# Kernel optimization log

Measured on AMD Instinct MI355X. Metric: run time of the kernel, lower is better.

## Reference

```python
import jax, jax.numpy as jnp
import numpy as np

V, E, H, T = 50000, 1024, 1024, 128
L, MAXL = 50, 50
PAD, O_TOK = 0, 1


def setup_inputs() -> dict:
    key = jax.random.key(0)
    ks = jax.random.split(key, 18)
    s = 0.05
    f = lambda k, shape: jax.random.normal(k, shape, jnp.float32) * s
    return {
        'input_ids': jax.random.randint(ks[0], (1, L), 1, V),
        'tag_ids': jax.random.randint(ks[1], (1, L), 1, T),  # >=1 so no pad tags
        'word_embed': f(ks[2], (V, E)),
        'enc_Wih': f(ks[3], (3 * H, E)),
        'enc_Whh': f(ks[4], (3 * H, H)),
        'enc_bih': f(ks[5], (3 * H,)),
        'enc_bhh': f(ks[6], (3 * H,)),
        'dec_embed': f(ks[7], (T, H)),
        'attn_W': f(ks[8], (MAXL, 2 * H)),
        'attn_b': f(ks[9], (MAXL,)),
        'comb_W': f(ks[10], (H, 2 * H)),
        'comb_b': f(ks[11], (H,)),
        'dec_Wih': f(ks[12], (3 * H, H)),
        'dec_Whh': f(ks[13], (3 * H, H)),
        'dec_bih': f(ks[14], (3 * H,)),
        'dec_bhh': f(ks[15], (3 * H,)),
        'out_W': f(ks[16], (T, H)),
        'out_b': f(ks[17], (T,)),
    }


def _gru_cell(x, h, Wih, Whh, bih, bhh):
    # PyTorch GRU cell semantics
    gi = Wih @ x + bih
    gh = Whh @ h + bhh
    i_r, i_z, i_n = jnp.split(gi, 3)
    h_r, h_z, h_n = jnp.split(gh, 3)
    r = jax.nn.sigmoid(i_r + h_r)
    z = jax.nn.sigmoid(i_z + h_z)
    n = jnp.tanh(i_n + r * h_n)
    return (1.0 - z) * n + z * h


def _forward(word_embed, enc_Wih, enc_Whh, enc_bih, enc_bhh,
             dec_embed, attn_W, attn_b, comb_W, comb_b,
             dec_Wih, dec_Whh, dec_bih, dec_bhh, out_W, out_b,
             input_ids, tag_ids):
    src = input_ids[0]  # (L,)
    tgt = tag_ids[0]    # (L,)

    def enc_step(h, tok):
        h2 = _gru_cell(word_embed[tok], h, enc_Wih, enc_Whh, enc_bih, enc_bhh)
        return h2, h2

    h_enc, enc_outs = jax.lax.scan(enc_step, jnp.zeros((H,), word_embed.dtype), src)
    # enc_outs: (L, H); L == MAX_LENGTH so the buffer is fully filled

    dec_in = jnp.concatenate([jnp.array([O_TOK], tgt.dtype), tgt[:-1]])  # teacher forcing

    def dec_step(h, xt):
        tok, tgt_t = xt
        e = dec_embed[tok]  # (H,), dropout is identity in eval
        aw = jax.nn.softmax(attn_W @ jnp.concatenate([e, h]) + attn_b)  # (MAXL,)
        ctx = aw @ enc_outs  # (H,)
        o = jax.nn.relu(comb_W @ jnp.concatenate([e, ctx]) + comb_b)
        h2 = _gru_cell(o, h, dec_Wih, dec_Whh, dec_bih, dec_bhh)
        logp = jax.nn.log_softmax(out_W @ h2 + out_b)  # decoder output (log-probs)
        # original applies CrossEntropyLoss on log-probs -> log_softmax applied twice
        nll = -jax.nn.log_softmax(logp)[tgt_t]
        step_loss = jnp.where(tgt_t == PAD, jnp.zeros((), logp.dtype), nll)
        return h2, (logp, step_loss)

    _, (logps, losses) = jax.lax.scan(dec_step, h_enc, (dec_in, tgt))
    return logps, jnp.sum(losses)  # (L, T), scalar


def reference(input_ids, tag_ids, word_embed, enc_Wih, enc_Whh, enc_bih, enc_bhh,
              dec_embed, attn_W, attn_b, comb_W, comb_b,
              dec_Wih, dec_Whh, dec_bih, dec_bhh, out_W, out_b):
    return _forward(word_embed, enc_Wih, enc_Whh, enc_bih, enc_bhh,
                    dec_embed, attn_W, attn_b, comb_W, comb_b,
                    dec_Wih, dec_Whh, dec_bih, dec_bhh, out_W, out_b,
                    input_ids, tag_ids)
```

## Files before the change

### kernel.cpp

```cpp
#include <hip/hip_runtime.h>
#include <cstdint>


#define HDIM 1024
#define LSEQ 50
#define TDIM 128
#define PB   6
#define NPROD 128
#define LSTRP 65

typedef float f32x4 __attribute__((ext_vector_type(4)));
typedef _Float16 h2 __attribute__((ext_vector_type(2)));

#if __has_builtin(__builtin_amdgcn_fdot2)
#define FDOT2(a,b,c) __builtin_amdgcn_fdot2((a),(b),(c),false)
#else
__device__ __forceinline__ float fdot2_sw(h2 a, h2 b, float c){
  return c + (float)a[0]*(float)b[0] + (float)a[1]*(float)b[1];
}
#define FDOT2(a,b,c) fdot2_sw((a),(b),(c))
#endif

struct KArgs {
  const int* input_ids; const int* tag_ids;
  const float* word_embed;
  const float* enc_Wih; const float* enc_Whh; const float* enc_bih; const float* enc_bhh;
  const float* dec_embed; const float* attn_W; const float* attn_b;
  const float* comb_W; const float* comb_b;
  const float* dec_Wih; const float* dec_Whh; const float* dec_bih; const float* dec_bhh;
  const float* out_W; const float* out_b;
  float* out;
  unsigned* ctrE; unsigned* ctrM; unsigned* ctrO; unsigned* ctrV;
  float* hbE;
  float* hbD;
  float* obD;
  float* logits;
  float* attn_e;
  float* pre_comb;
  float* MT;
  float* enc_outs;
};

__device__ __forceinline__ void fence_vm(){
  asm volatile("s_waitcnt vmcnt(0)" ::: "memory");
}
__device__ __forceinline__ void st_coh(float* p, float v){
  __hip_atomic_store(p, v, __ATOMIC_RELAXED, __HIP_MEMORY_SCOPE_AGENT);
}
__device__ __forceinline__ void st_tag(float* p, float v, unsigned tag){
  unsigned b = (__float_as_uint(v) & ~31u) | tag;
  st_coh(p, __uint_as_float(b));
}
__device__ __forceinline__ void stf(unsigned* p, unsigned v){
  __hip_atomic_store(p, v, __ATOMIC_RELAXED, __HIP_MEMORY_SCOPE_AGENT);
}
__device__ __forceinline__ unsigned ldu(const unsigned* p){
  return __hip_atomic_load(p, __ATOMIC_RELAXED, __HIP_MEMORY_SCOPE_AGENT);
}
__device__ __forceinline__ void addc(unsigned* base, int bid){
  __hip_atomic_fetch_add(base + (bid&7)*16, 1u, __ATOMIC_RELAXED, __HIP_MEMORY_SCOPE_AGENT);
}
__device__ __forceinline__ void addc0(unsigned* base){
  __hip_atomic_fetch_add(base, 1u, __ATOMIC_RELAXED, __HIP_MEMORY_SCOPE_AGENT);
}
__device__ __forceinline__ f32x4 coh_load4(const float* p){
  f32x4 v;
  asm volatile("global_load_dwordx4 %0, %1, off sc0 sc1\n\ts_waitcnt vmcnt(0)"
               : "=v"(v) : "v"(p) : "memory");
  return v;
}

template<int N>
__device__ __forceinline__ void wred_batch(float* v){
  #pragma unroll
  for(int o=32;o>0;o>>=1){
    #pragma unroll
    for(int i=0;i<N;i++) v[i] += __shfl_xor(v[i],o,64);
  }
}
__device__ __forceinline__ float wred_sum(float v){
  #pragma unroll
  for(int o=32;o>0;o>>=1) v += __shfl_xor(v,o,64);
  return v;
}
__device__ __forceinline__ float wred_max(float v){
  #pragma unroll
  for(int o=32;o>0;o>>=1) v = fmaxf(v,__shfl_xor(v,o,64));
  return v;
}

struct Chunk { f32x4 a,b,c,d; };
__device__ __forceinline__ Chunk load_chunk(const float* __restrict__ row, int lane){
  const f32x4* p = reinterpret_cast<const f32x4*>(row) + lane*4;
  Chunk w; w.a=p[0]; w.b=p[1]; w.c=p[2]; w.d=p[3]; return w;
}
__device__ __forceinline__ float chunk_dot(const Chunk& w, const float* hc){
  return w.a.x*hc[0]+w.a.y*hc[1]+w.a.z*hc[2]+w.a.w*hc[3]
       + w.b.x*hc[4]+w.b.y*hc[5]+w.b.z*hc[6]+w.b.w*hc[7]
       + w.c.x*hc[8]+w.c.y*hc[9]+w.c.z*hc[10]+w.c.w*hc[11]
       + w.d.x*hc[12]+w.d.y*hc[13]+w.d.z*hc[14]+w.d.w*hc[15];
}
__device__ __forceinline__ void load_vec16(const float* __restrict__ v, float* hc, int lane){
  const f32x4* p = reinterpret_cast<const f32x4*>(v) + lane*4;
  f32x4 x0=p[0],x1=p[1],x2=p[2],x3=p[3];
  hc[0]=x0.x; hc[1]=x0.y; hc[2]=x0.z; hc[3]=x0.w;
  hc[4]=x1.x; hc[5]=x1.y; hc[6]=x1.z; hc[7]=x1.w;
  hc[8]=x2.x; hc[9]=x2.y; hc[10]=x2.z; hc[11]=x2.w;
  hc[12]=x3.x; hc[13]=x3.y; hc[14]=x3.z; hc[15]=x3.w;
}

struct PChunk { unsigned m[8]; };
__device__ __forceinline__ h2 as_h2(unsigned u){ return __builtin_bit_cast(h2, u); }
__device__ __forceinline__ unsigned as_u(h2 h){ return __builtin_bit_cast(unsigned, h); }
__device__ __forceinline__ unsigned pack2(float a, float b){
  return as_u((h2){(_Float16)a, (_Float16)b});
}
__device__ __forceinline__ PChunk load_pchunk(const float* __restrict__ row, int lane){
  const f32x4* p = reinterpret_cast<const f32x4*>(row) + lane*4;
  f32x4 a=p[0],b=p[1],c=p[2],d=p[3];
  PChunk w;
  w.m[0]=pack2(a.x,a.y); w.m[1]=pack2(a.z,a.w);
  w.m[2]=pack2(b.x,b.y); w.m[3]=pack2(b.z,b.w);
  w.m[4]=pack2(c.x,c.y); w.m[5]=pack2(c.z,c.w);
  w.m[6]=pack2(d.x,d.y); w.m[7]=pack2(d.z,d.w);
  return w;
}
__device__ __forceinline__ void pinp(PChunk& c){
  asm volatile("" : "+v"(c.m[0]),"+v"(c.m[1]),"+v"(c.m[2]),"+v"(c.m[3]),
                    "+v"(c.m[4]),"+v"(c.m[5]),"+v"(c.m[6]),"+v"(c.m[7]));
}
__device__ __forceinline__ void pin32(unsigned& x){ asm volatile("" : "+v"(x)); }
__device__ __forceinline__ float pdot(const PChunk& w, const h2* hp){
  float acc = 0.f;
  #pragma unroll
  for(int k=0;k<8;k++) acc = FDOT2(as_h2(w.m[k]), hp[k], acc);
  return acc;
}
__device__ __forceinline__ float sigm(float x){ return 1.f/(1.f+expf(-x)); }
__device__ __forceinline__ void pack16(const float* ec, h2* ep){
  #pragma unroll
  for(int k=0;k<8;k++) ep[k]=(h2){(_Float16)ec[2*k],(_Float16)ec[2*k+1]};
}

template<int SLP>
__device__ __forceinline__ void stage_tag_p(h2* ldsp, const float* g, int tid, unsigned tag){
  const float* p = g + 4*tid;
  f32x4 v;
  for(;;){
    v = coh_load4(p);
    unsigned m = ((__float_as_uint(v.x)&31u)^tag) | ((__float_as_uint(v.y)&31u)^tag)
               | ((__float_as_uint(v.z)&31u)^tag) | ((__float_as_uint(v.w)&31u)^tag);
    if(m==0u) break;
    if(SLP) __builtin_amdgcn_s_sleep(SLP);
  }
  int q = tid>>2, m0 = (tid&3)*2;
  ldsp[m0*LSTRP+q]     = (h2){(_Float16)v.x,(_Float16)v.y};
  ldsp[(m0+1)*LSTRP+q] = (h2){(_Float16)v.z,(_Float16)v.w};
}
__device__ __forceinline__ void read8p(const h2* ldsp, h2* hp, int lane){
  #pragma unroll
  for(int k=0;k<8;k++) hp[k]=ldsp[k*LSTRP+lane];
}
__device__ __forceinline__ float hread(const h2* ldsp, int j){
  int pj = j>>1;
  h2 v = ldsp[(pj&7)*LSTRP + (pj>>3)];
  return (float)v[j&1];
}

__device__ __forceinline__ void wait8(const unsigned* base, unsigned n, int lane){
  const unsigned* p = base + lane*16;
  for(;;){
    unsigned v = (lane<8)? ldu(p) : 0xFFFFFFFFu;
    if(__all((int)(v>=n))) return;
    __builtin_amdgcn_s_sleep(8);
  }
}

__global__ __launch_bounds__(256,1) void seq2seq_kernel(KArgs A){
  const int bid = blockIdx.x, tid = threadIdx.x;
  const int wave = tid>>6, lane = tid&63;
  __shared__ h2 ldsp_h[8*LSTRP+8];
  __shared__ h2 ldsp_o[8*LSTRP+8];
  __shared__ h2 awpL[32];
  __shared__ float smr[64];
  __shared__ float smL[TDIM];
  __shared__ float smA[64];
  __shared__ float giL[LSEQ*24];

  const int gv = bid*4 + wave;

  const int p = bid - PB;
  const bool is_prod = (p>=0 && p<NPROD);
  const int base = is_prod ? p*8 : 0;
  const int j8 = base + (tid&7);

  if(is_prod){
    {
      PChunk wgi[6]; float bgi[6];
      #pragma unroll
      for(int i=0;i<6;i++){
        int r = wave + 4*i;
        int le=r/3, g=r-3*le, grow=g*HDIM+base+le;
        wgi[i] = load_pchunk(A.enc_Wih + (size_t)grow*HDIM, lane);
        pinp(wgi[i]);
        bgi[i] = A.enc_bih[grow];
      }
      for(int te=0;te<LSEQ;++te){
        int tok = A.input_ids[te];
        float ec[16]; load_vec16(A.word_embed + (size_t)tok*HDIM, ec, lane);
        h2 ep[8]; pack16(ec, ep);
        float d[6];
        #pragma unroll
        for(int i=0;i<6;i++) d[i]=pdot(wgi[i],ep);
        wred_batch<6>(d);
        if(lane==0){
          #pragma unroll
          for(int i=0;i<6;i++) giL[te*24 + wave+4*i] = d[i]+bgi[i];
        }
      }
      __syncthreads();
    }
    PChunk wep[6];
    #pragma unroll
    for(int i=0;i<6;i++){
      int r = wave + 4*i;
      int le=r/3, g=r-3*le, row=g*HDIM+base+le;
      wep[i] = load_pchunk(A.enc_Whh + (size_t)row*HDIM, lane);
      pinp(wep[i]);
    }
    float bh0=A.enc_bhh[j8], bh1=A.enc_bhh[HDIM+j8], bh2=A.enc_bhh[2*HDIM+j8];
    for(int te=0;te<LSEQ;++te){
      h2 hp[8];
      if(te>0){
        stage_tag_p<1>(ldsp_h, A.hbE + ((te-1)&1)*HDIM, tid, (unsigned)(te&31));
        __syncthreads();
        read8p(ldsp_h, hp, lane);
      } else {
        #pragma unroll
        for(int k=0;k<8;k++) hp[k]=(h2){(_Float16)0.f,(_Float16)0.f};
      }
      float part[6];
      #pragma unroll
      for(int i=0;i<6;i++) part[i]=pdot(wep[i],hp);
      wred_batch<6>(part);
      if(lane==0){
        #pragma unroll
        for(int i=0;i<6;i++) smr[wave+4*i]=part[i];
      }
      __syncthreads();
      if(tid<8){
        int j = base+tid;
        float gr=smr[tid*3]+bh0, gz=smr[tid*3+1]+bh1, gn=smr[tid*3+2]+bh2;
        float gi0=giL[te*24+3*tid], gi1=giL[te*24+3*tid+1], gi2=giL[te*24+3*tid+2];
        float hj = (te>0)? hread(ldsp_h, j) : 0.f;
        float r_=sigm(gi0+gr), z_=sigm(gi1+gz);
        float n_=tanhf(gi2+r_*gn);
        float h2v=(1.f-z_)*n_+z_*hj;
        st_tag(&A.hbE[(te&1)*HDIM+j], h2v, (unsigned)((te+1)&31));
        st_coh(&A.enc_outs[te*HDIM+j], h2v);
        if(te==LSEQ-1) st_tag(&A.hbD[j], h2v, 0u);
      }
      __syncthreads();
    }
    fence_vm();
    __syncthreads();
    if(tid==0) addc(A.ctrE, bid);
  } else {
    const int q = (bid<6)? bid : bid-128;
    PChunk wpc[2]; float bpc[2]; int ri[2];
    #pragma unroll
    for(int k=0;k<2;k++){
      ri[k] = q*8 + wave*2 + k;
      wpc[k] = load_pchunk(A.comb_W + (size_t)ri[k]*2*HDIM, lane);
      pinp(wpc[k]);
      bpc[k] = A.comb_b[ri[k]];
    }
    for(int t=0;t<LSEQ;++t){
      int tok = (t==0)?1:A.tag_ids[t-1];
      float ec[16]; load_vec16(A.dec_embed + (size_t)tok*HDIM, ec, lane);
      h2 ep[8]; pack16(ec, ep);
      float d[2] = {pdot(wpc[0],ep), pdot(wpc[1],ep)};
      wred_batch<2>(d);
      if(lane==0){
        st_coh(&A.pre_comb[t*HDIM+ri[0]], d[0]+bpc[0]);
        st_coh(&A.pre_comb[t*HDIM+ri[1]], d[1]+bpc[1]);
      }
    }
    if(q < LSEQ){
      PChunk wae = load_pchunk(A.attn_W + (size_t)q*2*HDIM, lane);
      float bae = A.attn_b[q];
      const int t0 = wave*13, tc = (wave<3)?13:11;
      for(int u=0;u<tc;++u){
        int t = t0+u;
        int tok = (t==0)?1:A.tag_ids[t-1];
        float ec[16]; load_vec16(A.dec_embed + (size_t)tok*HDIM, ec, lane);
        h2 ep[8]; pack16(ec, ep);
        float d = wred_sum(pdot(wae,ep));
        if(lane==0) st_coh(&A.attn_e[t*LSEQ+q], d+bae);
      }
    }
    fence_vm();
    __syncthreads();
  }

  if(wave==0) wait8(A.ctrE, 16u, lane);
  __syncthreads();
  {
    Chunk wm = load_chunk(A.comb_W + (size_t)gv*2*HDIM + HDIM, lane);
    for(int sg=0;sg<10;++sg){
      float pt[5];
      #pragma unroll
      for(int j=0;j<5;j++){
        float ec[16]; load_vec16(A.enc_outs + (sg*5+j)*HDIM, ec, lane);
        pt[j]=chunk_dot(wm,ec);
      }
      wred_batch<5>(pt);
      if(lane==0){
        #pragma unroll
        for(int j=0;j<5;j++) st_coh(&A.MT[(sg*5+j)*HDIM+gv], pt[j]);
      }
    }
  }
  fence_vm();
  __syncthreads();
  if(tid==0) addc(A.ctrM, bid);
  {
    const bool keep = is_prod || bid<5 || (bid>=134 && bid<150);
    if(!keep) return;
  }
  if(wave==0) wait8(A.ctrM, 32u, lane);
  __syncthreads();

  if(bid < 4){
    const int oi = bid*256 + tid;
    PChunk wa13[13];
    int srow[13];
    #pragma unroll
    for(int i=0;i<13;i++){
      int s = wave + 4*i; int sc = (s<LSEQ)? s : 0;
      wa13[i] = load_pchunk(A.attn_W + (size_t)sc*2*HDIM + HDIM, lane);
      pinp(wa13[i]);
      srow[i] = s;
    }
    unsigned mp[25];
    #pragma unroll
    for(int k=0;k<25;k++){
      mp[k] = pack2(A.MT[(2*k)*HDIM+oi], A.MT[(2*k+1)*HDIM+oi]);
      pin32(mp[k]);
    }
    for(int t=0;t<LSEQ;++t){
      const unsigned tg = (unsigned)(t&31);
      float ae[13];
      #pragma unroll
      for(int i=0;i<13;i++)
        ae[i] = (srow[i]<LSEQ)? A.attn_e[t*LSEQ+srow[i]] : 0.f;
      float pcv = A.pre_comb[t*HDIM+oi];
      stage_tag_p<1>(ldsp_h, A.hbD + (t%3)*HDIM, tid, tg);
      __syncthreads();
      h2 hp[8]; read8p(ldsp_h, hp, lane);
      float pl[13];
      #pragma unroll
      for(int i=0;i<13;i++) pl[i]=pdot(wa13[i],hp);
      wred_batch<13>(pl);
      if(lane==0){
        #pragma unroll
        for(int i=0;i<13;i++) if(srow[i]<LSEQ) smL[srow[i]]=pl[i]+ae[i];
      }
      __syncthreads();
      if(wave==0){
        float l = (lane<LSEQ)? smL[lane] : -1e30f;
        float m = wred_max(l);
        float pe = (lane<LSEQ)? expf(l-m) : 0.f;
        float ss = wred_sum(pe);
        if(lane<LSEQ) smA[lane] = pe/ss;
      }
      __syncthreads();
      if(tid<25) awpL[tid] = (h2){(_Float16)smA[2*tid],(_Float16)smA[2*tid+1]};
      __syncthreads();
      float acc = pcv;
      #pragma unroll
      for(int k=0;k<25;k++) acc = FDOT2(as_h2(mp[k]), awpL[k], acc);
      st_tag(&A.obD[(t&1)*HDIM+oi], fmaxf(acc,0.f), tg);
      __syncthreads();
    }
  } else if(bid == 4){
    float loss = 0.f;
    for(int t=0;t<LSEQ;++t){
      if(tid<32){
        const float* pp = A.logits + (t&1)*TDIM + 4*tid;
        const unsigned tg = (unsigned)(t&31);
        f32x4 v;
        for(;;){
          v = coh_load4(pp);
          unsigned m = ((__float_as_uint(v.x)&31u)^tg) | ((__float_as_uint(v.y)&31u)^tg)
                     | ((__float_as_uint(v.z)&31u)^tg) | ((__float_as_uint(v.w)&31u)^tg);
          if(m==0u) break;
          __builtin_amdgcn_s_sleep(2);
        }
        smL[4*tid]=v.x; smL[4*tid+1]=v.y; smL[4*tid+2]=v.z; smL[4*tid+3]=v.w;
      }
      __syncthreads();
      if(tid==0) stf(A.ctrV, (unsigned)(t+1));
      if(wave==0){
        float l0=smL[lane], l1=smL[lane+64];
        float m  = wred_max(fmaxf(l0,l1));
        float pe = expf(l0-m)+expf(l1-m);
        float s1 = wred_sum(pe);
        float lse = m + logf(s1);
        float lp0 = l0-lse, lp1 = l1-lse;
        float m2  = wred_max(fmaxf(lp0,lp1));
        float p2  = expf(lp0-m2)+expf(lp1-m2);
        float s2  = wred_sum(p2);
        float lse2 = m2 + logf(s2);
        A.out[t*TDIM + lane]      = lp0;
        A.out[t*TDIM + 64 + lane] = lp1;
        int tg2 = A.tag_ids[t];
        float c = ((lane==tg2)?(lse2-lp0):0.f) + ((lane+64==tg2)?(lse2-lp1):0.f);
        c = wred_sum(c);
        if(tg2 != 0) loss += c;
      }
      __syncthreads();
    }
    if(tid==0) A.out[LSEQ*TDIM] = loss;
  } else if(is_prod){
    PChunk whp[6], wip[6];
    #pragma unroll
    for(int i=0;i<6;i++){
      int r = wave + 4*i;
      int le=r/3, g=r-3*le, row=g*HDIM+base+le;
      whp[i] = load_pchunk(A.dec_Whh + (size_t)row*HDIM, lane);
      pinp(whp[i]);
      wip[i] = load_pchunk(A.dec_Wih + (size_t)row*HDIM, lane);
      pinp(wip[i]);
    }
    float dh0=A.dec_bhh[j8], dh1=A.dec_bhh[HDIM+j8], dh2=A.dec_bhh[2*HDIM+j8];
    float di0=A.dec_bih[j8], di1=A.dec_bih[HDIM+j8], di2=A.dec_bih[2*HDIM+j8];
    for(int t=0;t<LSEQ;++t){
      const unsigned tg = (unsigned)(t&31);
      stage_tag_p<1>(ldsp_h, A.hbD + (t%3)*HDIM, tid, tg);
      __syncthreads();
      h2 hp[8]; read8p(ldsp_h, hp, lane);
      float ph[6];
      #pragma unroll
      for(int i=0;i<6;i++) ph[i]=pdot(whp[i],hp);
      wred_batch<6>(ph);
      if(lane==0){
        #pragma unroll
        for(int i=0;i<6;i++) smr[wave+4*i]=ph[i];
      }
      if(wave==0 && t>=3){
        const unsigned tgt = 16u*(unsigned)(t-2);
        for(;;){
          unsigned v = (lane==0)? ldu(A.ctrO) : tgt;
          if(__all((int)(v>=tgt))) break;
          __builtin_amdgcn_s_sleep(2);
        }
      }
      stage_tag_p<1>(ldsp_o, A.obD + (t&1)*HDIM, tid, tg);
      __syncthreads();
      h2 op[8]; read8p(ldsp_o, op, lane);
      float po[6];
      #pragma unroll
      for(int i=0;i<6;i++) po[i]=pdot(wip[i],op);
      wred_batch<6>(po);
      if(lane==0){
        #pragma unroll
        for(int i=0;i<6;i++) smr[32+wave+4*i]=po[i];
      }
      __syncthreads();
      if(tid<8){
        int j = base+tid;
        float gr=smr[tid*3]+dh0,    gz=smr[tid*3+1]+dh1,    gn=smr[tid*3+2]+dh2;
        float ir=smr[32+tid*3]+di0, iz=smr[32+tid*3+1]+di1, inn=smr[32+tid*3+2]+di2;
        float hj = hread(ldsp_h, j);
        float r_=sigm(ir+gr), z_=sigm(iz+gz);
        float n_=tanhf(inn+r_*gn);
        float h2v=(1.f-z_)*n_+z_*hj;
        st_tag(&A.hbD[((t+1)%3)*HDIM+j], h2v, (unsigned)((t+1)&31));
      }
      __syncthreads();
    }
  } else {
    const int ob = bid-134;
    PChunk wop[2];
    float bo[2];
    #pragma unroll
    for(int i=0;i<2;i++){
      int row = ob*8 + wave*2 + i;
      wop[i]=load_pchunk(A.out_W+(size_t)row*HDIM,lane);
      pinp(wop[i]);
      bo[i]=A.out_b[row];
    }
    for(int t=0;t<LSEQ;++t){
      const unsigned tg1 = (unsigned)((t+1)&31);
      stage_tag_p<2>(ldsp_h, A.hbD + ((t+1)%3)*HDIM, tid, tg1);
      __syncthreads();
      if(tid==0) addc0(A.ctrO);
      h2 hp[8]; read8p(ldsp_h, hp, lane);
      float pt[2]={pdot(wop[0],hp),pdot(wop[1],hp)};
      wred_batch<2>(pt);
      if(wave==0 && t>=2){
        const unsigned tgt = (unsigned)(t-1);
        for(;;){
          unsigned v = (lane==0)? ldu(A.ctrV) : tgt;
          if(__all((int)(v>=tgt))) break;
          __builtin_amdgcn_s_sleep(4);
        }
      }
      __syncthreads();
      if(lane==0){
        int row = ob*8 + wave*2;
        st_tag(&A.logits[(t&1)*TDIM + row],   pt[0]+bo[0], (unsigned)(t&31));
        st_tag(&A.logits[(t&1)*TDIM + row+1], pt[1]+bo[1], (unsigned)(t&31));
      }
      __syncthreads();
    }
  }
}

extern "C" void kernel_launch(void* const* d_in, const int* in_sizes, int n_in,
                              void* d_out, int out_size, void* d_ws, size_t ws_size,
                              hipStream_t stream){
  (void)in_sizes; (void)n_in; (void)out_size; (void)ws_size;
  KArgs A;
  A.input_ids = (const int*)d_in[0];
  A.tag_ids   = (const int*)d_in[1];
  A.word_embed= (const float*)d_in[2];
  A.enc_Wih   = (const float*)d_in[3];
  A.enc_Whh   = (const float*)d_in[4];
  A.enc_bih   = (const float*)d_in[5];
  A.enc_bhh   = (const float*)d_in[6];
  A.dec_embed = (const float*)d_in[7];
  A.attn_W    = (const float*)d_in[8];
  A.attn_b    = (const float*)d_in[9];
  A.comb_W    = (const float*)d_in[10];
  A.comb_b    = (const float*)d_in[11];
  A.dec_Wih   = (const float*)d_in[12];
  A.dec_Whh   = (const float*)d_in[13];
  A.dec_bih   = (const float*)d_in[14];
  A.dec_bhh   = (const float*)d_in[15];
  A.out_W     = (const float*)d_in[16];
  A.out_b     = (const float*)d_in[17];
  A.out       = (float*)d_out;

  unsigned* u = (unsigned*)d_ws;
  A.ctrE = u;
  A.ctrM = u + 128;
  A.ctrO = u + 256;
  A.ctrV = u + 320;
  float* f = (float*)d_ws + 1024;
  A.hbE    = f; f += 2*HDIM;
  A.hbD    = f; f += 3*HDIM;
  A.obD    = f; f += 2*HDIM;
  A.logits = f; f += 2*TDIM;
  A.attn_e   = f; f += LSEQ*LSEQ + 14;
  A.pre_comb = f; f += LSEQ*HDIM;
  A.MT       = f; f += LSEQ*HDIM;
  A.enc_outs = f; f += LSEQ*HDIM;

  (void)hipMemsetAsync(d_ws, 0, 4096, stream);
  (void)hipMemsetAsync((char*)d_ws + 4096, 0xFF, 7424*4, stream);
  void* args[] = { &A };
  hipError_t err = hipLaunchCooperativeKernel((const void*)seq2seq_kernel,
                                              dim3(256), dim3(256), args, 0, stream);
  if(err != hipSuccess){
    hipLaunchKernelGGL(seq2seq_kernel, dim3(256), dim3(256), 0, stream, A);
  }
}
```

Baseline: 463.9 us.

## Overlap encoder-output projection with encoder recurrence via tagged streaming

Removes the grid-wide barrier after the encoder that the MT = comb_W[:,H:] @ enc_outs projection used to wait on. Encoder outputs are now written with per-step tags, and the 128 non-producer blocks project each timestep as soon as its tagged row becomes visible. That work runs in parallel with the encoder recurrence instead of after it. Only the attention blocks wait on a single counter for MT completion. The cost is a larger memset to initialize the tags and fp16 rounding of enc_outs in the projection.

```diff
diff --git a/kernel.cpp b/kernel.cpp
--- a/kernel.cpp
+++ b/kernel.cpp
@@ -30,15 +30,15 @@
   const float* dec_Wih; const float* dec_Whh; const float* dec_bih; const float* dec_bhh;
   const float* out_W; const float* out_b;
   float* out;
-  unsigned* ctrE; unsigned* ctrM; unsigned* ctrO; unsigned* ctrV;
+  unsigned* ctrM; unsigned* ctrO; unsigned* ctrV;
   float* hbE;
   float* hbD;
   float* obD;
   float* logits;
+  float* enc_outs;
   float* attn_e;
   float* pre_comb;
   float* MT;
-  float* enc_outs;
 };
 
 __device__ __forceinline__ void fence_vm(){
@@ -56,9 +56,6 @@
 }
 __device__ __forceinline__ unsigned ldu(const unsigned* p){
   return __hip_atomic_load(p, __ATOMIC_RELAXED, __HIP_MEMORY_SCOPE_AGENT);
-}
-__device__ __forceinline__ void addc(unsigned* base, int bid){
-  __hip_atomic_fetch_add(base + (bid&7)*16, 1u, __ATOMIC_RELAXED, __HIP_MEMORY_SCOPE_AGENT);
 }
 __device__ __forceinline__ void addc0(unsigned* base){
   __hip_atomic_fetch_add(base, 1u, __ATOMIC_RELAXED, __HIP_MEMORY_SCOPE_AGENT);
@@ -89,17 +86,6 @@
   return v;
 }
 
-struct Chunk { f32x4 a,b,c,d; };
-__device__ __forceinline__ Chunk load_chunk(const float* __restrict__ row, int lane){
-  const f32x4* p = reinterpret_cast<const f32x4*>(row) + lane*4;
-  Chunk w; w.a=p[0]; w.b=p[1]; w.c=p[2]; w.d=p[3]; return w;
-}
-__device__ __forceinline__ float chunk_dot(const Chunk& w, const float* hc){
-  return w.a.x*hc[0]+w.a.y*hc[1]+w.a.z*hc[2]+w.a.w*hc[3]
-       + w.b.x*hc[4]+w.b.y*hc[5]+w.b.z*hc[6]+w.b.w*hc[7]
-       + w.c.x*hc[8]+w.c.y*hc[9]+w.c.z*hc[10]+w.c.w*hc[11]
-       + w.d.x*hc[12]+w.d.y*hc[13]+w.d.z*hc[14]+w.d.w*hc[15];
-}
 __device__ __forceinline__ void load_vec16(const float* __restrict__ v, float* hc, int lane){
   const f32x4* p = reinterpret_cast<const f32x4*>(v) + lane*4;
   f32x4 x0=p[0],x1=p[1],x2=p[2],x3=p[3];
@@ -167,12 +153,40 @@
   return (float)v[j&1];
 }
 
-__device__ __forceinline__ void wait8(const unsigned* base, unsigned n, int lane){
-  const unsigned* p = base + lane*16;
+__device__ __forceinline__ void wait2_enc(const float* g, unsigned tg, int lane){
+  const float* p0 = g + lane*16 + 7;
+  const float* p1 = g + lane*16 + 15;
   for(;;){
-    unsigned v = (lane<8)? ldu(p) : 0xFFFFFFFFu;
-    if(__all((int)(v>=n))) return;
-    __builtin_amdgcn_s_sleep(8);
+    float a,b;
+    asm volatile("global_load_dword %0, %2, off sc0 sc1\n\t"
+                 "global_load_dword %1, %3, off sc0 sc1\n\t"
+                 "s_waitcnt vmcnt(0)"
+                 : "=v"(a), "=v"(b) : "v"(p0), "v"(p1) : "memory");
+    unsigned m = ((__float_as_uint(a)&31u)^tg) | ((__float_as_uint(b)&31u)^tg);
+    if(__all((int)(m==0u))) return;
+    __builtin_amdgcn_s_sleep(4);
+  }
+}
+__device__ __forceinline__ void load16_tag(const float* g, unsigned tg, int lane, h2* ep){
+  const float* p = g + lane*16;
+  for(;;){
+    f32x4 a=coh_load4(p), b=coh_load4(p+4), c=coh_load4(p+8), d=coh_load4(p+12);
+    unsigned m = ((__float_as_uint(a.x)&31u)^tg)|((__float_as_uint(a.y)&31u)^tg)
+               | ((__float_as_uint(a.z)&31u)^tg)|((__float_as_uint(a.w)&31u)^tg)
+               | ((__float_as_uint(b.x)&31u)^tg)|((__float_as_uint(b.y)&31u)^tg)
+               | ((__float_as_uint(b.z)&31u)^tg)|((__float_as_uint(b.w)&31u)^tg)
+               | ((__float_as_uint(c.x)&31u)^tg)|((__float_as_uint(c.y)&31u)^tg)
+               | ((__float_as_uint(c.z)&31u)^tg)|((__float_as_uint(c.w)&31u)^tg)
+               | ((__float_as_uint(d.x)&31u)^tg)|((__float_as_uint(d.y)&31u)^tg)
+               | ((__float_as_uint(d.z)&31u)^tg)|((__float_as_uint(d.w)&31u)^tg);
+    if(m==0u){
+      ep[0]=(h2){(_Float16)a.x,(_Float16)a.y}; ep[1]=(h2){(_Float16)a.z,(_Float16)a.w};
+      ep[2]=(h2){(_Float16)b.x,(_Float16)b.y}; ep[3]=(h2){(_Float16)b.z,(_Float16)b.w};
+      ep[4]=(h2){(_Float16)c.x,(_Float16)c.y}; ep[5]=(h2){(_Float16)c.z,(_Float16)c.w};
+      ep[6]=(h2){(_Float16)d.x,(_Float16)d.y}; ep[7]=(h2){(_Float16)d.z,(_Float16)d.w};
+      return;
+    }
+    __builtin_amdgcn_s_sleep(2);
   }
 }
 
@@ -186,8 +200,6 @@
   __shared__ float smL[TDIM];
   __shared__ float smA[64];
   __shared__ float giL[LSEQ*24];
-
-  const int gv = bid*4 + wave;
 
   const int p = bid - PB;
   const bool is_prod = (p>=0 && p<NPROD);
@@ -257,14 +269,13 @@
         float n_=tanhf(gi2+r_*gn);
         float h2v=(1.f-z_)*n_+z_*hj;
         st_tag(&A.hbE[(te&1)*HDIM+j], h2v, (unsigned)((te+1)&31));
-        st_coh(&A.enc_outs[te*HDIM+j], h2v);
+        st_tag(&A.enc_outs[te*HDIM+j], h2v, (unsigned)(te%31));
         if(te==LSEQ-1) st_tag(&A.hbD[j], h2v, 0u);
       }
       __syncthreads();
     }
     fence_vm();
     __syncthreads();
-    if(tid==0) addc(A.ctrE, bid);
   } else {
     const int q = (bid<6)? bid : bid-128;
     PChunk wpc[2]; float bpc[2]; int ri[2];
@@ -299,37 +310,29 @@
         if(lane==0) st_coh(&A.attn_e[t*LSEQ+q], d+bae);
       }
     }
+    {
+      const int si = q*4 + wave;
+      PChunk wm0 = load_pchunk(A.comb_W + (size_t)si*2*HDIM + HDIM, lane);
+      pinp(wm0);
+      PChunk wm1 = load_pchunk(A.comb_W + (size_t)(si+512)*2*HDIM + HDIM, lane);
+      pinp(wm1);
+      for(int s=0;s<LSEQ;++s){
+        const unsigned tg = (unsigned)(s%31);
+        const float* g = A.enc_outs + s*HDIM;
+        wait2_enc(g, tg, lane);
+        h2 ep[8]; load16_tag(g, tg, lane, ep);
+        float dd[2] = {pdot(wm0,ep), pdot(wm1,ep)};
+        wred_batch<2>(dd);
+        if(lane==0){
+          st_coh(&A.MT[s*HDIM+si],     dd[0]);
+          st_coh(&A.MT[s*HDIM+si+512], dd[1]);
+        }
+      }
+    }
     fence_vm();
     __syncthreads();
-  }
-
-  if(wave==0) wait8(A.ctrE, 16u, lane);
-  __syncthreads();
-  {
-    Chunk wm = load_chunk(A.comb_W + (size_t)gv*2*HDIM + HDIM, lane);
-    for(int sg=0;sg<10;++sg){
-      float pt[5];
-      #pragma unroll
-      for(int j=0;j<5;j++){
-        float ec[16]; load_vec16(A.enc_outs + (sg*5+j)*HDIM, ec, lane);
-        pt[j]=chunk_dot(wm,ec);
-      }
-      wred_batch<5>(pt);
-      if(lane==0){
-        #pragma unroll
-        for(int j=0;j<5;j++) st_coh(&A.MT[(sg*5+j)*HDIM+gv], pt[j]);
-      }
-    }
-  }
-  fence_vm();
-  __syncthreads();
-  if(tid==0) addc(A.ctrM, bid);
-  {
-    const bool keep = is_prod || bid<5 || (bid>=134 && bid<150);
-    if(!keep) return;
-  }
-  if(wave==0) wait8(A.ctrM, 32u, lane);
-  __syncthreads();
+    if(tid==0) addc0(A.ctrM);
+  }
 
   if(bid < 4){
     const int oi = bid*256 + tid;
@@ -342,6 +345,14 @@
       pinp(wa13[i]);
       srow[i] = s;
     }
+    if(wave==0){
+      for(;;){
+        unsigned v = (lane==0)? ldu(A.ctrM) : 128u;
+        if(__all((int)(v>=128u))) break;
+        __builtin_amdgcn_s_sleep(2);
+      }
+    }
+    __syncthreads();
     unsigned mp[25];
     #pragma unroll
     for(int k=0;k<25;k++){
@@ -480,7 +491,7 @@
       }
       __syncthreads();
     }
-  } else {
+  } else if(bid>=134 && bid<150){
     const int ob = bid-134;
     PChunk wop[2];
     float bo[2];
@@ -544,22 +555,21 @@
   A.out       = (float*)d_out;
 
   unsigned* u = (unsigned*)d_ws;
-  A.ctrE = u;
-  A.ctrM = u + 128;
-  A.ctrO = u + 256;
-  A.ctrV = u + 320;
+  A.ctrM = u;
+  A.ctrO = u + 64;
+  A.ctrV = u + 128;
   float* f = (float*)d_ws + 1024;
-  A.hbE    = f; f += 2*HDIM;
-  A.hbD    = f; f += 3*HDIM;
-  A.obD    = f; f += 2*HDIM;
-  A.logits = f; f += 2*TDIM;
+  A.hbE      = f; f += 2*HDIM;
+  A.hbD      = f; f += 3*HDIM;
+  A.obD      = f; f += 2*HDIM;
+  A.logits   = f; f += 2*TDIM;
+  A.enc_outs = f; f += LSEQ*HDIM;
   A.attn_e   = f; f += LSEQ*LSEQ + 14;
   A.pre_comb = f; f += LSEQ*HDIM;
   A.MT       = f; f += LSEQ*HDIM;
-  A.enc_outs = f; f += LSEQ*HDIM;
 
   (void)hipMemsetAsync(d_ws, 0, 4096, stream);
-  (void)hipMemsetAsync((char*)d_ws + 4096, 0xFF, 7424*4, stream);
+  (void)hipMemsetAsync((char*)d_ws + 4096, 0xFF, 58624*4, stream);
   void* args[] = { &A };
   hipError_t err = hipLaunchCooperativeKernel((const void*)seq2seq_kernel,
                                               dim3(256), dim3(256), args, 0, stream);
```

Result: no change. 458.8 us (-1.1%).
